# Kernel tuning notes

Hardware: AMD Instinct MI355X
Metric: run time of the kernel (lower is better)

Reference implementation:

```python
import jax, jax.numpy as jnp
import numpy as np

BN_EPS = 1e-5


def _bn_train(x, gamma, beta):
    # torch BatchNorm1d in training mode: normalize with batch mean and
    # biased batch variance.
    mu = jnp.mean(x, axis=0)
    var = jnp.var(x, axis=0)
    return (x - mu) * jax.lax.rsqrt(var + BN_EPS) * gamma + beta


def setup_inputs() -> dict:
    key = jax.random.key(0)
    ks = jax.random.split(key, 12)
    N, F_D, F_C, E, VOCAB, H = 16384, 26, 10, 16, 200000, 400
    D_IN = (F_D + F_C) * E  # 576
    return {
        "Xi_dense": jax.random.normal(ks[0], (N, F_D, 1), jnp.float32),
        "Xv": jax.random.uniform(ks[1], (N, F_D + F_C), jnp.float32),
        "Wd": jax.random.normal(ks[2], (F_D, E), jnp.float32) * 0.1,
        "bd": jax.random.normal(ks[3], (F_D, E), jnp.float32) * 0.1,
        "tables": jax.random.normal(ks[4], (F_C, VOCAB, E), jnp.float32) * 0.1,
        "W1": jax.random.normal(ks[5], (H, D_IN), jnp.float32) * 0.05,
        "b1": jax.random.normal(ks[6], (H,), jnp.float32) * 0.05,
        "g1": jnp.ones((H,), jnp.float32),
        "be1": jnp.zeros((H,), jnp.float32),
        "W2": jax.random.normal(ks[7], (H, H), jnp.float32) * 0.05,
        "b2": jax.random.normal(ks[8], (H,), jnp.float32) * 0.05,
        "g2": jnp.ones((H,), jnp.float32),
        "be2": jnp.zeros((H,), jnp.float32),
        "bias_vec": jax.random.normal(ks[9], (N,), jnp.float32),
        "Xi_cat": jax.random.randint(ks[10], (N, F_C, 1), 0, VOCAB, jnp.int32),
    }


def reference(Xi_dense, Xv, Wd, bd, tables, W1, b1, g1, be1,
              W2, b2, g2, be2, bias_vec, Xi_cat):
    N = Xi_dense.shape[0]
    # dense fields: per-field Linear(1, E) -> x * W + b, shape (N, 26, E)
    dense_emb = Xi_dense * Wd[None] + bd[None]  # (N,26,1)*(1,26,E) broadcast
    # categorical fields: per-field embedding lookup, shape (N, 10, E)
    cat_emb = jax.vmap(lambda tbl, idx: tbl[idx], in_axes=(0, 1), out_axes=1)(
        tables, Xi_cat[:, :, 0])
    # scale each field embedding by its Xv value
    all_emb = jnp.concatenate([dense_emb, cat_emb], axis=1) * Xv[:, :, None]  # (N,36,E)

    # fm first order: concat of all scaled field embeddings
    fm_first = all_emb.reshape(N, -1)  # (N, 576)
    # fm second order: 0.5 * ((sum)^2 - sum of squares)
    s = jnp.sum(all_emb, axis=1)                       # (N, E)
    fm_second = 0.5 * (s * s - jnp.sum(all_emb * all_emb, axis=1))  # (N, E)

    # deep part: Linear -> BatchNorm (train-mode stats) per hidden layer;
    # dropout p=0 -> identity.
    deep = fm_first
    deep = _bn_train(deep @ W1.T + b1, g1, be1)
    deep = _bn_train(deep @ W2.T + b2, g2, be2)

    total = (jnp.sum(fm_first, axis=1) + jnp.sum(fm_second, axis=1)
             + jnp.sum(deep, axis=1) + bias_vec)
    return total
```

## Files before the change

### kernel.cpp

```cpp
#include <hip/hip_runtime.h>

#define BN_EPS 1e-5f

typedef unsigned short u16;
typedef __attribute__((ext_vector_type(8))) short bf16x8;
typedef __attribute__((ext_vector_type(4))) float f32x4;

__device__ __forceinline__ u16 f2bf(float x) {
  union { float f; unsigned int u; } v; v.f = x;
  unsigned int r = v.u + 0x7fffu + ((v.u >> 16) & 1u);
  return (u16)(r >> 16);
}
__device__ __forceinline__ float bf2f(u16 h) {
  union { unsigned int u; float f; } v; v.u = ((unsigned int)h) << 16;
  return v.f;
}

__device__ __forceinline__ float wave_reduce_sum(float v) {
#pragma unroll
  for (int off = 1; off < 64; off <<= 1) v += __shfl_xor(v, off, 64);
  return v;
}

__device__ __forceinline__ void gload_lds16(const void* g, void* l) {
  __builtin_amdgcn_global_load_lds(
      (const __attribute__((address_space(1))) void*)g,
      (__attribute__((address_space(3))) void*)l, 16, 0, 0);
}

__global__ __launch_bounds__(256) void embed_prep(
    const float* __restrict__ Xi_dense, const float* __restrict__ Xv,
    const float* __restrict__ Wd, const float* __restrict__ bd,
    const float* __restrict__ tables, const int* __restrict__ Xi_cat,
    const float* __restrict__ bias_vec, const float* __restrict__ W1,
    u16* __restrict__ fm_first, float* __restrict__ partial,
    u16* __restrict__ W1h, float* __restrict__ statz) {
  const int t = threadIdx.x;
  if (blockIdx.x >= 512) {
    const int bb = blockIdx.x - 512;
    if (bb == 0) {
#pragma unroll
      for (int i = 0; i < 8; ++i) statz[i * 256 + t] = 0.f;
    }
    const int base = bb * 4096;
#pragma unroll
    for (int e = 0; e < 16; ++e) {
      const int idx = base + e * 256 + t;
      const int r = idx / 576;
      const int j = idx - r * 576;
      W1h[idx] = (r < 400) ? f2bf(W1[r * 576 + j]) : (u16)0;
    }
    return;
  }

  __shared__ float Xvs[32 * 37];
  __shared__ float Xds[32 * 27];
  __shared__ int Cis[32 * 11];
  __shared__ float Wds[416], Bds[416];
  const int n0 = blockIdx.x * 32;

  for (int i = t; i < 1152; i += 256) {
    const int r = i / 36;
    Xvs[r * 37 + (i - r * 36)] = Xv[n0 * 36 + i];
  }
  for (int i = t; i < 832; i += 256) {
    const int r = i / 26;
    Xds[r * 27 + (i - r * 26)] = Xi_dense[n0 * 26 + i];
  }
  for (int i = t; i < 320; i += 256) {
    const int r = i / 10;
    Cis[r * 11 + (i - r * 10)] = Xi_cat[n0 * 10 + i];
  }
  for (int i = t; i < 416; i += 256) {
    Wds[i] = Wd[i];
    Bds[i] = bd[i];
  }
  __syncthreads();

  const int r = t >> 3, q = t & 7;
  const int n = n0 + r;
  const int fbase = q >> 1, eh = (q & 1) * 8;
  float s8[8] = {}, q8[8] = {};
  float sum_all = 0.f;
  u16* frow = fm_first + (size_t)n * 576;

#pragma unroll
  for (int j = 0; j < 9; ++j) {
    const int f = fbase + 4 * j;
    const float xvv = Xvs[r * 37 + f];
    float val[8];
    if (f < 26) {
      const float xd = Xds[r * 27 + f];
      const float4 w0 = *(const float4*)&Wds[f * 16 + eh];
      const float4 w1 = *(const float4*)&Wds[f * 16 + eh + 4];
      const float4 b0 = *(const float4*)&Bds[f * 16 + eh];
      const float4 b1v = *(const float4*)&Bds[f * 16 + eh + 4];
      val[0] = fmaf(xd, w0.x, b0.x) * xvv;
      val[1] = fmaf(xd, w0.y, b0.y) * xvv;
      val[2] = fmaf(xd, w0.z, b0.z) * xvv;
      val[3] = fmaf(xd, w0.w, b0.w) * xvv;
      val[4] = fmaf(xd, w1.x, b1v.x) * xvv;
      val[5] = fmaf(xd, w1.y, b1v.y) * xvv;
      val[6] = fmaf(xd, w1.z, b1v.z) * xvv;
      val[7] = fmaf(xd, w1.w, b1v.w) * xvv;
    } else {
      const int fc = f - 26;
      const int row = Cis[r * 11 + fc];
      const float* tp =
          tables + ((size_t)fc * 200000 + (size_t)row) * 16 + eh;
      const float4 v0 = *(const float4*)tp;
      const float4 v1 = *(const float4*)(tp + 4);
      val[0] = v0.x * xvv;
      val[1] = v0.y * xvv;
      val[2] = v0.z * xvv;
      val[3] = v0.w * xvv;
      val[4] = v1.x * xvv;
      val[5] = v1.y * xvv;
      val[6] = v1.z * xvv;
      val[7] = v1.w * xvv;
    }
    bf16x8 o;
#pragma unroll
    for (int jj = 0; jj < 8; ++jj) {
      s8[jj] += val[jj];
      q8[jj] += val[jj] * val[jj];
      sum_all += val[jj];
      o[jj] = (short)f2bf(val[jj]);
    }
    *(bf16x8*)&frow[f * 16 + eh] = o;
  }

  float fm2h = 0.f;
#pragma unroll
  for (int jj = 0; jj < 8; ++jj) {
    float se = s8[jj] + __shfl_xor(s8[jj], 2, 64);
    se += __shfl_xor(se, 4, 64);
    float qe = q8[jj] + __shfl_xor(q8[jj], 2, 64);
    qe += __shfl_xor(qe, 4, 64);
    fm2h += se * se - qe;
  }
  const float fm2 = 0.5f * (fm2h + __shfl_xor(fm2h, 1, 64));
  float srow = sum_all + __shfl_xor(sum_all, 1, 64);
  srow += __shfl_xor(srow, 2, 64);
  srow += __shfl_xor(srow, 4, 64);
  if (q == 0) partial[n] = srow + fm2 + bias_vec[n];
}

template <int NFR>
__device__ __forceinline__ void gemm_body(
    const u16* __restrict__ A, int lda, const u16* __restrict__ W, int ldw,
    u16* __restrict__ Y, int ldc, int Ncap, float* __restrict__ aS,
    float* __restrict__ aQ, int K, int bx, int by, u16* As, u16* Bs,
    float (&rS)[2][4][2][16], float (&rQ)[2][4][2][16]) {
  const int t = threadIdx.x;
  const int bm = bx * 64;
  const int bn = by * 128;
  const int wid = t >> 6, lane = t & 63;
  const int wr = wid >> 1, wc = wid & 1;
  const int lr = lane & 15, lk = (lane >> 4) * 8;
  const int sr = lane >> 2;
  const int sk = (lane & 3) * 8;
  const bool active = (NFR == 4) || (wc == 0);

  f32x4 acc[2][NFR] = {};

  for (int kt = 0; kt < K; kt += 32) {
    gload_lds16(&A[(size_t)(bm + wid * 16 + sr) * lda + kt + sk],
                &As[wid * 512]);
#pragma unroll
    for (int i = 0; i < 2; ++i) {
      const int c = wid * 2 + i;
      if (NFR == 4 || c < 2)
        gload_lds16(&W[(size_t)(bn + c * 16 + sr) * ldw + kt + sk],
                    &Bs[c * 512]);
    }
    __syncthreads();

    if (active) {
      bf16x8 af[2], bfv[NFR];
#pragma unroll
      for (int mf = 0; mf < 2; ++mf)
        af[mf] = *(const bf16x8*)&As[(wr * 32 + mf * 16 + lr) * 32 + lk];
#pragma unroll
      for (int nf = 0; nf < NFR; ++nf)
        bfv[nf] = *(const bf16x8*)&Bs[(wc * 64 + nf * 16 + lr) * 32 + lk];
#pragma unroll
      for (int mf = 0; mf < 2; ++mf)
#pragma unroll
        for (int nf = 0; nf < NFR; ++nf)
          acc[mf][nf] = __builtin_amdgcn_mfma_f32_16x16x32_bf16(
              af[mf], bfv[nf], acc[mf][nf], 0, 0, 0);
    }
    __syncthreads();
  }

  const int l4 = (lane >> 4) * 4;
  if (active) {
#pragma unroll
    for (int nf = 0; nf < NFR; ++nf) {
      const int col = bn + wc * 64 + nf * 16 + lr;
      float s = 0.f, q = 0.f;
#pragma unroll
      for (int mf = 0; mf < 2; ++mf) {
#pragma unroll
        for (int r = 0; r < 4; ++r) {
          const int row = bm + wr * 32 + mf * 16 + l4 + r;
          const float v = acc[mf][nf][r];
          s += v;
          q += v * v;
          if (col < Ncap) Y[(size_t)row * ldc + col] = f2bf(v);
        }
      }
      s += __shfl_xor(s, 16, 64);
      s += __shfl_xor(s, 32, 64);
      q += __shfl_xor(q, 16, 64);
      q += __shfl_xor(q, 32, 64);
      if (lane < 16) {
        rS[wc][nf][wr][lr] = s;
        rQ[wc][nf][wr][lr] = q;
      }
    }
  }
  __syncthreads();
  if (t < (NFR == 4 ? 128 : 32)) {
    const int wcc = t >> 6, nff = (t >> 4) & 3, c = t & 15;
    atomicAdd(&aS[bn + t], rS[wcc][nff][0][c] + rS[wcc][nff][1][c]);
    atomicAdd(&aQ[bn + t], rQ[wcc][nff][0][c] + rQ[wcc][nff][1][c]);
  }
}

__global__ __launch_bounds__(256) void gemm_bf16(
    const u16* __restrict__ A, int lda,
    const u16* __restrict__ W, int ldw,
    u16* __restrict__ Y, int ldc, int Ncap,
    float* __restrict__ aS, float* __restrict__ aQ, int K) {
  __shared__ u16 As[64 * 32];
  __shared__ u16 Bs[128 * 32];
  __shared__ float rS[2][4][2][16];
  __shared__ float rQ[2][4][2][16];
  const int bid = blockIdx.x;
  const int l = (bid & 7) * (gridDim.x >> 3) + (bid >> 3);
  const int bx = l >> 2, by = l & 3;
  if (by < 3)
    gemm_body<4>(A, lda, W, ldw, Y, ldc, Ncap, aS, aQ, K, bx, by, As, Bs,
                 rS, rQ);
  else
    gemm_body<2>(A, lda, W, ldw, Y, ldc, Ncap, aS, aQ, K, bx, by, As, Bs,
                 rS, rQ);
}

__global__ __launch_bounds__(256) void prep2(
    const float* __restrict__ aS1, const float* __restrict__ aQ1,
    const float* __restrict__ g1, const float* __restrict__ W2,
    u16* __restrict__ W2p) {
  const int c = blockIdx.x * 256 + threadIdx.x;
  const int row = c / 104;
  const int jc = (c - row * 104) * 4;
  ushort4 o = {0, 0, 0, 0};
  if (row < 400 && jc < 400) {
    const float4 S = *(const float4*)&aS1[jc];
    const float4 Q = *(const float4*)&aQ1[jc];
    const float4 G = *(const float4*)&g1[jc];
    const float4 w = *(const float4*)&W2[(size_t)row * 400 + jc];
    const float inv = 1.f / 16384.f;
    float mu, var, a;
    mu = S.x * inv; var = Q.x * inv - mu * mu;
    a = G.x * rsqrtf(var + BN_EPS); o.x = f2bf(w.x * a);
    mu = S.y * inv; var = Q.y * inv - mu * mu;
    a = G.y * rsqrtf(var + BN_EPS); o.y = f2bf(w.y * a);
    mu = S.z * inv; var = Q.z * inv - mu * mu;
    a = G.z * rsqrtf(var + BN_EPS); o.z = f2bf(w.z * a);
    mu = S.w * inv; var = Q.w * inv - mu * mu;
    a = G.w * rsqrtf(var + BN_EPS); o.w = f2bf(w.w * a);
  }
  *(ushort4*)&W2p[(size_t)row * 416 + jc] = o;
}

__device__ __forceinline__ void bn_affine4(const float* aS, const float* aQ,
                                           const float* g, const float* be,
                                           int j, float4& aa, float4& cc) {
  const float4 S = *(const float4*)&aS[j];
  const float4 Q = *(const float4*)&aQ[j];
  const float4 G = *(const float4*)&g[j];
  const float4 E = *(const float4*)&be[j];
  const float inv = 1.f / 16384.f;
  float mu, var;
  mu = S.x * inv; var = Q.x * inv - mu * mu;
  aa.x = G.x * rsqrtf(var + BN_EPS); cc.x = E.x - mu * aa.x;
  mu = S.y * inv; var = Q.y * inv - mu * mu;
  aa.y = G.y * rsqrtf(var + BN_EPS); cc.y = E.y - mu * aa.y;
  mu = S.z * inv; var = Q.z * inv - mu * mu;
  aa.z = G.z * rsqrtf(var + BN_EPS); cc.z = E.z - mu * aa.z;
  mu = S.w * inv; var = Q.w * inv - mu * mu;
  aa.w = G.w * rsqrtf(var + BN_EPS); cc.w = E.w - mu * aa.w;
}

__global__ __launch_bounds__(256) void final_kernel(
    const u16* __restrict__ Y2, const float* __restrict__ aS2,
    const float* __restrict__ aQ2, const float* __restrict__ g2,
    const float* __restrict__ be2, const float* __restrict__ partial,
    float* __restrict__ out) {
  const int t = threadIdx.x;
  const int lane = t & 63;
  const int wid = t >> 6;
  const int j0 = lane * 8;
  float ar[8], cr[8];
  if (j0 < 400) {
    float4 aa0, cc0, aa1, cc1;
    bn_affine4(aS2, aQ2, g2, be2, j0, aa0, cc0);
    bn_affine4(aS2, aQ2, g2, be2, j0 + 4, aa1, cc1);
    ar[0] = aa0.x; ar[1] = aa0.y; ar[2] = aa0.z; ar[3] = aa0.w;
    ar[4] = aa1.x; ar[5] = aa1.y; ar[6] = aa1.z; ar[7] = aa1.w;
    cr[0] = cc0.x; cr[1] = cc0.y; cr[2] = cc0.z; cr[3] = cc0.w;
    cr[4] = cc1.x; cr[5] = cc1.y; cr[6] = cc1.z; cr[7] = cc1.w;
  } else {
#pragma unroll
    for (int k = 0; k < 8; ++k) { ar[k] = 0.f; cr[k] = 0.f; }
  }
#pragma unroll
  for (int r = 0; r < 4; ++r) {
    const int n = blockIdx.x * 16 + wid * 4 + r;
    float acc = 0.f;
    if (j0 < 400) {
      const bf16x8 y = *(const bf16x8*)&Y2[(size_t)n * 400 + j0];
#pragma unroll
      for (int k = 0; k < 8; ++k)
        acc += fmaf(ar[k], bf2f((u16)y[k]), cr[k]);
    }
    acc = wave_reduce_sum(acc);
    if (lane == 0) out[n] = partial[n] + acc;
  }
}

extern "C" void kernel_launch(void* const* d_in, const int* in_sizes, int n_in,
                              void* d_out, int out_size, void* d_ws,
                              size_t ws_size, hipStream_t stream) {
  const float* Xi_dense = (const float*)d_in[0];
  const float* Xv = (const float*)d_in[1];
  const float* Wd = (const float*)d_in[2];
  const float* bd = (const float*)d_in[3];
  const float* tables = (const float*)d_in[4];
  const float* W1 = (const float*)d_in[5];
  const float* g1 = (const float*)d_in[7];
  const float* W2 = (const float*)d_in[9];
  const float* g2 = (const float*)d_in[11];
  const float* be2 = (const float*)d_in[12];
  const float* bias_vec = (const float*)d_in[13];
  const int* Xi_cat = (const int*)d_in[14];

  constexpr int N = 16384;
  constexpr int DIN = 576;
  constexpr int H = 400;
  constexpr int KP = 416;
  constexpr int WPAD = 512;
  constexpr int NXB = 256;

  u16* fm_first = (u16*)d_ws;
  u16* Y1h = fm_first + (size_t)N * DIN;
  u16* Y2h = Y1h + (size_t)N * KP;
  u16* W1h = Y2h + (size_t)N * H;
  u16* W2p = W1h + (size_t)WPAD * DIN;
  float* fptr = (float*)(W2p + (size_t)WPAD * KP);
  float* partial = fptr;
  float* aS1 = partial + N;
  float* aQ1 = aS1 + WPAD;
  float* aS2 = aQ1 + WPAD;
  float* aQ2 = aS2 + WPAD;

  embed_prep<<<512 + 72, 256, 0, stream>>>(Xi_dense, Xv, Wd, bd, tables,
                                           Xi_cat, bias_vec, W1, fm_first,
                                           partial, W1h, aS1);

  gemm_bf16<<<NXB * 4, 256, 0, stream>>>(fm_first, DIN, W1h, DIN,
                                         Y1h, KP, KP, aS1, aQ1, DIN);

  prep2<<<208, 256, 0, stream>>>(aS1, aQ1, g1, W2, W2p);

  gemm_bf16<<<NXB * 4, 256, 0, stream>>>(Y1h, KP, W2p, KP,
                                         Y2h, H, H, aS2, aQ2, KP);

  final_kernel<<<N / 16, 256, 0, stream>>>(Y2h, aS2, aQ2, g2, be2, partial,
                                           (float*)d_out);
}
```

Baseline: 65.27 us.

## Double-buffer GEMM LDS tiles to overlap global loads with MFMA compute

Converts the GEMM main loop to a two-stage LDS ping-pong: the next K tile is issued via direct-to-LDS loads while the current tile is consumed, with a partial vmcnt wait and raw barriers replacing two full syncthreads per iteration. It also raises wave priority around the MFMA block and changes the NFR=2 path so every wave issues loads (possibly redundant duplicate writes of the same rows). It doubles LDS usage for the tiles, which may reduce occupancy, and relies on the hand-counted vmcnt(3) matching the number of outstanding loads per stage.

Result: slower. 67.36 us (+3.2%).

```diff
diff --git a/kernel.cpp b/kernel.cpp
--- a/kernel.cpp
+++ b/kernel.cpp
@@ -150,8 +150,9 @@
 __device__ __forceinline__ void gemm_body(
     const u16* __restrict__ A, int lda, const u16* __restrict__ W, int ldw,
     u16* __restrict__ Y, int ldc, int Ncap, float* __restrict__ aS,
-    float* __restrict__ aQ, int K, int bx, int by, u16* As, u16* Bs,
-    float (&rS)[2][4][2][16], float (&rQ)[2][4][2][16]) {
+    float* __restrict__ aQ, int K, int bx, int by, u16 (*As)[64 * 32],
+    u16 (*Bs)[128 * 32], float (&rS)[2][4][2][16],
+    float (&rQ)[2][4][2][16]) {
   const int t = threadIdx.x;
   const int bm = bx * 64;
   const int bn = by * 128;
@@ -164,37 +165,53 @@
 
   f32x4 acc[2][NFR] = {};
 
-  for (int kt = 0; kt < K; kt += 32) {
+  auto STAGE = [&](int buf, int kt) {
     gload_lds16(&A[(size_t)(bm + wid * 16 + sr) * lda + kt + sk],
-                &As[wid * 512]);
+                &As[buf][wid * 512]);
 #pragma unroll
     for (int i = 0; i < 2; ++i) {
-      const int c = wid * 2 + i;
-      if (NFR == 4 || c < 2)
-        gload_lds16(&W[(size_t)(bn + c * 16 + sr) * ldw + kt + sk],
-                    &Bs[c * 512]);
-    }
-    __syncthreads();
-
+      const int c = (NFR == 4) ? (wid * 2 + i) : i;
+      gload_lds16(&W[(size_t)(bn + c * 16 + sr) * ldw + kt + sk],
+                  &Bs[buf][c * 512]);
+    }
+  };
+
+  auto COMPUTE = [&](int buf) {
     if (active) {
       bf16x8 af[2], bfv[NFR];
 #pragma unroll
       for (int mf = 0; mf < 2; ++mf)
-        af[mf] = *(const bf16x8*)&As[(wr * 32 + mf * 16 + lr) * 32 + lk];
+        af[mf] = *(const bf16x8*)&As[buf][(wr * 32 + mf * 16 + lr) * 32 + lk];
 #pragma unroll
       for (int nf = 0; nf < NFR; ++nf)
-        bfv[nf] = *(const bf16x8*)&Bs[(wc * 64 + nf * 16 + lr) * 32 + lk];
+        bfv[nf] = *(const bf16x8*)&Bs[buf][(wc * 64 + nf * 16 + lr) * 32 + lk];
+      __builtin_amdgcn_s_setprio(1);
 #pragma unroll
       for (int mf = 0; mf < 2; ++mf)
 #pragma unroll
         for (int nf = 0; nf < NFR; ++nf)
           acc[mf][nf] = __builtin_amdgcn_mfma_f32_16x16x32_bf16(
               af[mf], bfv[nf], acc[mf][nf], 0, 0, 0);
-    }
-    __syncthreads();
-  }
+      __builtin_amdgcn_s_setprio(0);
+    }
+  };
+
+  STAGE(0, 0);
+  int cur = 0;
+  for (int kt = 32; kt < K; kt += 32) {
+    STAGE(cur ^ 1, kt);
+    asm volatile("s_waitcnt vmcnt(3)" ::: "memory");
+    __builtin_amdgcn_s_barrier();
+    COMPUTE(cur);
+    __builtin_amdgcn_s_barrier();
+    cur ^= 1;
+  }
+  asm volatile("s_waitcnt vmcnt(0)" ::: "memory");
+  __builtin_amdgcn_s_barrier();
+  COMPUTE(cur);
 
   const int l4 = (lane >> 4) * 4;
+  __syncthreads();
   if (active) {
 #pragma unroll
     for (int nf = 0; nf < NFR; ++nf) {
@@ -234,8 +251,8 @@
     const u16* __restrict__ W, int ldw,
     u16* __restrict__ Y, int ldc, int Ncap,
     float* __restrict__ aS, float* __restrict__ aQ, int K) {
-  __shared__ u16 As[64 * 32];
-  __shared__ u16 Bs[128 * 32];
+  __shared__ u16 As[2][64 * 32];
+  __shared__ u16 Bs[2][128 * 32];
   __shared__ float rS[2][4][2][16];
   __shared__ float rQ[2][4][2][16];
   const int bid = blockIdx.x;
```
